# Kernel optimization log

Measured on AMD Instinct MI355X. Metric: run time of the kernel, lower is better.

## Reference

```python
import jax, jax.numpy as jnp
import numpy as np

N_HEADS = 8
EPS = 1e-5

def _mha(q_in, kv_in, wq, bq, wk, bk, wv, bv, wo, bo, causal):
    B, N, D = q_in.shape
    Dh = D // N_HEADS
    # projections (weights stored [in, out])
    Q = (q_in @ wq + bq).reshape(B, N, N_HEADS, Dh).swapaxes(1, 2)  # [B,H,N,Dh]
    K = (kv_in @ wk + bk).reshape(B, N, N_HEADS, Dh).swapaxes(1, 2)
    V = (kv_in @ wv + bv).reshape(B, N, N_HEADS, Dh).swapaxes(1, 2)
    scores = jnp.einsum('bhqd,bhkd->bhqk', Q, K) / jnp.sqrt(jnp.asarray(Dh, q_in.dtype))
    if causal:
        m = jnp.triu(jnp.ones((N, N), dtype=bool), k=1)
        scores = jnp.where(m, jnp.asarray(-jnp.inf, scores.dtype), scores)
    w = jax.nn.softmax(scores, axis=-1)
    attn = jnp.einsum('bhqk,bhkd->bhqd', w, V).swapaxes(1, 2).reshape(B, N, D)
    return attn @ wo + bo

def _ln(x, g, b):
    mu = jnp.mean(x, axis=-1, keepdims=True)
    var = jnp.var(x, axis=-1, keepdims=True)
    return (x - mu) / jnp.sqrt(var + EPS) * g + b

def setup_inputs() -> dict:
    key = jax.random.key(0)
    D, H, S = 512, 8, 4
    ks = jax.random.split(key, 32)
    def w(k, shape):
        return jax.random.normal(k, shape, dtype=jnp.float32) * 0.02
    inp = {
        'x': jax.random.normal(ks[0], (2, 2048, D), dtype=jnp.float32),
        'encoder_output': jax.random.normal(ks[1], (2, 2048, D), dtype=jnp.float32),
        # masked self-attention params
        'm_wq': w(ks[2], (D, D)), 'm_bq': jnp.zeros((D,), jnp.float32),
        'm_wk': w(ks[3], (D, D)), 'm_bk': jnp.zeros((D,), jnp.float32),
        'm_wv': w(ks[4], (D, D)), 'm_bv': jnp.zeros((D,), jnp.float32),
        'm_wo': w(ks[5], (D, D)), 'm_bo': jnp.zeros((D,), jnp.float32),
        # cross-attention params
        'c_wq': w(ks[6], (D, D)), 'c_bq': jnp.zeros((D,), jnp.float32),
        'c_wk': w(ks[7], (D, D)), 'c_bk': jnp.zeros((D,), jnp.float32),
        'c_wv': w(ks[8], (D, D)), 'c_bv': jnp.zeros((D,), jnp.float32),
        'c_wo': w(ks[9], (D, D)), 'c_bo': jnp.zeros((D,), jnp.float32),
        # layer norms
        'ln1_g': jnp.ones((D,), jnp.float32), 'ln1_b': jnp.zeros((D,), jnp.float32),
        'ln2_g': jnp.ones((D,), jnp.float32), 'ln2_b': jnp.zeros((D,), jnp.float32),
        'ln3_g': jnp.ones((D,), jnp.float32), 'ln3_b': jnp.zeros((D,), jnp.float32),
        # feed-forward (scale=4)
        'ff_w1': w(ks[10], (D, S * D)), 'ff_b1': jnp.zeros((S * D,), jnp.float32),
        'ff_w2': w(ks[11], (S * D, D)), 'ff_b2': jnp.zeros((D,), jnp.float32),
    }
    return inp

def reference(x, encoder_output,
              m_wq, m_bq, m_wk, m_bk, m_wv, m_bv, m_wo, m_bo,
              c_wq, c_bq, c_wk, c_bk, c_wv, c_bv, c_wo, c_bo,
              ln1_g, ln1_b, ln2_g, ln2_b, ln3_g, ln3_b,
              ff_w1, ff_b1, ff_w2, ff_b2):
    x = _mha(x, x, m_wq, m_bq, m_wk, m_bk, m_wv, m_bv, m_wo, m_bo, causal=True) + x
    x = _ln(x, ln1_g, ln1_b)
    x = _mha(x, encoder_output, c_wq, c_bq, c_wk, c_bk, c_wv, c_bv, c_wo, c_bo, causal=False) + x
    x = _ln(x, ln2_g, ln2_b)
    h = jax.nn.gelu(x @ ff_w1 + ff_b1, approximate=False)  # torch nn.GELU default = exact erf
    x = h @ ff_w2 + ff_b2 + x
    x = _ln(x, ln3_g, ln3_b)
    return x
```

## Files before the change

### kernel.cpp

```cpp
#include <hip/hip_runtime.h>
#include <hip/hip_bf16.h>

typedef __attribute__((ext_vector_type(8))) short short8;
typedef __attribute__((ext_vector_type(4))) float floatx4;
typedef unsigned short u16;
typedef unsigned int u32;

#define QSCALE 0.1803368801111244f

__device__ __forceinline__ u16 f2b(float f) {
    union { float f; u32 u; } v; v.f = f;
    u32 r = v.u + 0x7fffu + ((v.u >> 16) & 1u);
    return (u16)(r >> 16);
}

__device__ __forceinline__ float b2f(u16 b) {
    u32 u = ((u32)b) << 16;
    union { u32 u; float f; } v; v.u = u;
    return v.f;
}

__device__ __forceinline__ u32 pk2(float a, float b) {
    __hip_bfloat162 w = __float22bfloat162_rn(make_float2(a, b));
    return *(u32*)&w;
}

__device__ __forceinline__ float gelu_fast(float v) {
    float u = v * (0.7978845608028654f + 0.03567740814183367f * v * v);
    float t = exp2f(fminf(2.8853900817779268f * u, 80.f));
    return v * t * __builtin_amdgcn_rcpf(t + 1.f);
}

__device__ __forceinline__ void gload(const u16* g, u16* l) {
    __builtin_amdgcn_global_load_lds((const __attribute__((address_space(1))) void*)g,
                                     (__attribute__((address_space(3))) void*)l, 16, 0, 0);
}

struct TPent { const float* s; u16* d; int O; int dI; };
struct TP16 { TPent e[16]; };
__global__ __launch_bounds__(256) void transpose_convert16(TP16 p) {
    __shared__ float t[32][33];
    TPent e = p.e[blockIdx.z];
    int o0 = blockIdx.x * 32, i0 = blockIdx.y * 32;
    int tx = threadIdx.x, ty = threadIdx.y;
#pragma unroll
    for (int k = 0; k < 32; k += 8) t[ty + k][tx] = e.s[(size_t)(i0 + ty + k) * e.O + o0 + tx];
    __syncthreads();
#pragma unroll
    for (int k = 0; k < 32; k += 8) e.d[(size_t)(o0 + ty + k) * e.dI + i0 + tx] = f2b(t[tx][ty + k]);
}

__global__ __launch_bounds__(256) void gather_bias(const float* b0, const float* b1, const float* b2,
                                                   const float* b3, const float* b4,
                                                   float* dqkv, float* dkv) {
    int i = blockIdx.x * 256 + threadIdx.x;
    if      (i < 512)  dqkv[i] = b0[i];
    else if (i < 1024) dqkv[i] = b1[i - 512];
    else if (i < 1536) dqkv[i] = b2[i - 1024];
    else if (i < 2048) dkv[i - 1536] = b3[i - 1536];
    else               dkv[i - 1536] = b4[i - 2048];
}

__global__ __launch_bounds__(256) void cvt_bf16_2(const float4* __restrict__ s0, ushort4* __restrict__ d0,
                                                  const float4* __restrict__ s1, ushort4* __restrict__ d1) {
    int i = blockIdx.x * 256 + threadIdx.x;
    float4 v = s0[i];
    ushort4 o; o.x = f2b(v.x); o.y = f2b(v.y); o.z = f2b(v.z); o.w = f2b(v.w);
    d0[i] = o;
    v = s1[i];
    o.x = f2b(v.x); o.y = f2b(v.y); o.z = f2b(v.z); o.w = f2b(v.w);
    d1[i] = o;
}

__global__ __launch_bounds__(256) void gemm64x128(
    const u16* __restrict__ A, int lda,
    const u16* __restrict__ B, int ldb,
    int K,
    const float* __restrict__ bias,
    const float* __restrict__ residual,
    float* __restrict__ out_f, u16* __restrict__ out_b,
    int out_stride, int scale_ncols, int gelu_flag)
{
    __shared__ u16 lA[64 * 64];
    __shared__ u16 lB[128 * 64];
    int tid = threadIdx.x, wave = tid >> 6, lane = tid & 63;
    int g4 = lane >> 4, c16 = lane & 15;
    int swz = (c16 & 7) << 3;
    int bm = blockIdx.x * 64, bn = blockIdx.y * 128;
    int wm = (wave >> 1) * 32, wn = (wave & 1) * 64;
    int srow = tid >> 3, skseg = ((tid & 7) * 8) ^ ((srow & 7) << 3);
    const u16* Ar = A + (size_t)(bm + srow) * lda + skseg;
    const u16* Br = B + (size_t)(bn + srow) * ldb + skseg;
    size_t a32 = (size_t)32 * lda, b32 = (size_t)32 * ldb;

    floatx4 acc[2][4];
#pragma unroll
    for (int i = 0; i < 2; i++)
#pragma unroll
        for (int j = 0; j < 4; j++) acc[i][j] = (floatx4){0.f, 0.f, 0.f, 0.f};

    for (int kt = 0; kt < K; kt += 64) {
        __syncthreads();
        gload(Ar + kt,           lA + wave * 512);
        gload(Ar + kt + a32,     lA + 2048 + wave * 512);
        gload(Br + kt,           lB + wave * 512);
        gload(Br + kt + b32,     lB + 2048 + wave * 512);
        gload(Br + kt + 2 * b32, lB + 4096 + wave * 512);
        gload(Br + kt + 3 * b32, lB + 6144 + wave * 512);
        __syncthreads();
        short8 aF[2][2], bF[2][4];
#pragma unroll
        for (int kk = 0; kk < 2; kk++) {
            int ko = (g4 * 8 + kk * 32) ^ swz;
#pragma unroll
            for (int i = 0; i < 2; i++) aF[kk][i] = *(const short8*)&lA[(wm + i * 16 + c16) * 64 + ko];
#pragma unroll
            for (int j = 0; j < 4; j++) bF[kk][j] = *(const short8*)&lB[(wn + j * 16 + c16) * 64 + ko];
        }
#pragma unroll
        for (int kk = 0; kk < 2; kk++)
#pragma unroll
            for (int i = 0; i < 2; i++)
#pragma unroll
                for (int j = 0; j < 4; j++)
                    acc[i][j] = __builtin_amdgcn_mfma_f32_16x16x32_bf16(aF[kk][i], bF[kk][j], acc[i][j], 0, 0, 0);
    }

#pragma unroll
    for (int i = 0; i < 2; i++) {
        int row0 = bm + wm + i * 16 + g4 * 4;
#pragma unroll
        for (int j = 0; j < 4; j++) {
            int col = bn + wn + j * 16 + c16;
            float bv = bias[col];
#pragma unroll
            for (int r = 0; r < 4; r++) {
                int row = row0 + r;
                float v = acc[i][j][r] + bv;
                if (col < scale_ncols) v *= QSCALE;
                if (gelu_flag) v = gelu_fast(v);
                if (residual) v += residual[(size_t)row * out_stride + col];
                if (out_f) out_f[(size_t)row * out_stride + col] = v;
                else       out_b[(size_t)row * out_stride + col] = f2b(v);
            }
        }
    }
}

__global__ __launch_bounds__(256) void gemm64x128_dual(
    const u16* __restrict__ A0, const u16* __restrict__ B0, const float* __restrict__ bias0,
    u16* __restrict__ out0, int ostride0, int scale0,
    const u16* __restrict__ A1, const u16* __restrict__ B1, const float* __restrict__ bias1,
    u16* __restrict__ out1, int ostride1,
    int ys, int K, int lda, int ldb)
{
    __shared__ u16 lA[64 * 64];
    __shared__ u16 lB[128 * 64];
    int tid = threadIdx.x, wave = tid >> 6, lane = tid & 63;
    int g4 = lane >> 4, c16 = lane & 15;
    int swz = (c16 & 7) << 3;
    int by = blockIdx.y;
    const u16* A; const u16* B; const float* bias; u16* out; int ostride, scaleN, bn;
    if (by < ys) { A = A0; B = B0; bias = bias0; out = out0; ostride = ostride0; scaleN = scale0; bn = by * 128; }
    else         { A = A1; B = B1; bias = bias1; out = out1; ostride = ostride1; scaleN = 0;      bn = (by - ys) * 128; }
    int bm = blockIdx.x * 64;
    int wm = (wave >> 1) * 32, wn = (wave & 1) * 64;
    int srow = tid >> 3, skseg = ((tid & 7) * 8) ^ ((srow & 7) << 3);
    const u16* Ar = A + (size_t)(bm + srow) * lda + skseg;
    const u16* Br = B + (size_t)(bn + srow) * ldb + skseg;
    size_t a32 = (size_t)32 * lda, b32 = (size_t)32 * ldb;

    floatx4 acc[2][4];
#pragma unroll
    for (int i = 0; i < 2; i++)
#pragma unroll
        for (int j = 0; j < 4; j++) acc[i][j] = (floatx4){0.f, 0.f, 0.f, 0.f};

    for (int kt = 0; kt < K; kt += 64) {
        __syncthreads();
        gload(Ar + kt,           lA + wave * 512);
        gload(Ar + kt + a32,     lA + 2048 + wave * 512);
        gload(Br + kt,           lB + wave * 512);
        gload(Br + kt + b32,     lB + 2048 + wave * 512);
        gload(Br + kt + 2 * b32, lB + 4096 + wave * 512);
        gload(Br + kt + 3 * b32, lB + 6144 + wave * 512);
        __syncthreads();
        short8 aF[2][2], bF[2][4];
#pragma unroll
        for (int kk = 0; kk < 2; kk++) {
            int ko = (g4 * 8 + kk * 32) ^ swz;
#pragma unroll
            for (int i = 0; i < 2; i++) aF[kk][i] = *(const short8*)&lA[(wm + i * 16 + c16) * 64 + ko];
#pragma unroll
            for (int j = 0; j < 4; j++) bF[kk][j] = *(const short8*)&lB[(wn + j * 16 + c16) * 64 + ko];
        }
#pragma unroll
        for (int kk = 0; kk < 2; kk++)
#pragma unroll
            for (int i = 0; i < 2; i++)
#pragma unroll
                for (int j = 0; j < 4; j++)
                    acc[i][j] = __builtin_amdgcn_mfma_f32_16x16x32_bf16(aF[kk][i], bF[kk][j], acc[i][j], 0, 0, 0);
    }

#pragma unroll
    for (int i = 0; i < 2; i++) {
        int row0 = bm + wm + i * 16 + g4 * 4;
#pragma unroll
        for (int j = 0; j < 4; j++) {
            int col = bn + wn + j * 16 + c16;
            float bv = bias[col];
#pragma unroll
            for (int r = 0; r < 4; r++) {
                float v = acc[i][j][r] + bv;
                if (col < scaleN) v *= QSCALE;
                out[(size_t)(row0 + r) * ostride + col] = f2b(v);
            }
        }
    }
}

__global__ __launch_bounds__(256) void gemm64x64(
    const u16* __restrict__ A, int lda,
    const u16* __restrict__ B, int ldb,
    int K,
    const float* __restrict__ bias,
    u16* __restrict__ out_b,
    int out_stride, int scale_ncols)
{
    __shared__ u16 lA[64 * 64];
    __shared__ u16 lB[64 * 64];
    int tid = threadIdx.x, wave = tid >> 6, lane = tid & 63;
    int g4 = lane >> 4, c16 = lane & 15;
    int swz = (c16 & 7) << 3;
    int bm = blockIdx.x * 64, bn = blockIdx.y * 64;
    int wm = wave * 16;
    int srow = tid >> 3, skseg = ((tid & 7) * 8) ^ ((srow & 7) << 3);
    const u16* Ar = A + (size_t)(bm + srow) * lda + skseg;
    const u16* Br = B + (size_t)(bn + srow) * ldb + skseg;
    size_t a32 = (size_t)32 * lda, b32 = (size_t)32 * ldb;

    floatx4 acc[4];
#pragma unroll
    for (int j = 0; j < 4; j++) acc[j] = (floatx4){0.f, 0.f, 0.f, 0.f};

    for (int kt = 0; kt < K; kt += 64) {
        __syncthreads();
        gload(Ar + kt,       lA + wave * 512);
        gload(Ar + kt + a32, lA + 2048 + wave * 512);
        gload(Br + kt,       lB + wave * 512);
        gload(Br + kt + b32, lB + 2048 + wave * 512);
        __syncthreads();
        short8 aF[2], bF[2][4];
#pragma unroll
        for (int kk = 0; kk < 2; kk++) {
            int ko = (g4 * 8 + kk * 32) ^ swz;
            aF[kk] = *(const short8*)&lA[(wm + c16) * 64 + ko];
#pragma unroll
            for (int j = 0; j < 4; j++) bF[kk][j] = *(const short8*)&lB[(j * 16 + c16) * 64 + ko];
        }
#pragma unroll
        for (int kk = 0; kk < 2; kk++)
#pragma unroll
            for (int j = 0; j < 4; j++)
                acc[j] = __builtin_amdgcn_mfma_f32_16x16x32_bf16(aF[kk], bF[kk][j], acc[j], 0, 0, 0);
    }

    int row0 = bm + wm + g4 * 4;
#pragma unroll
    for (int j = 0; j < 4; j++) {
        int col = bn + j * 16 + c16;
        float bv = bias[col];
#pragma unroll
        for (int r = 0; r < 4; r++) {
            int row = row0 + r;
            float v = acc[j][r] + bv;
            if (col < scale_ncols) v *= QSCALE;
            out_b[(size_t)row * out_stride + col] = f2b(v);
        }
    }
}

__global__ __launch_bounds__(256) void gemm64x64s(
    const u16* __restrict__ A, int lda,
    const u16* __restrict__ B, int ldb,
    int Ksub,
    const float* __restrict__ bias,
    const float* __restrict__ res_f,
    const u16* __restrict__ res_b,
    u16* __restrict__ out0, int out_stride)
{
    __shared__ u16 lA[64 * 64];
    __shared__ u16 lB[64 * 64];
    int tid = threadIdx.x, wave = tid >> 6, lane = tid & 63;
    int g4 = lane >> 4, c16 = lane & 15;
    int swz = (c16 & 7) << 3;
    int bm = blockIdx.x * 64, bn = blockIdx.y * 64, sp = blockIdx.z;
    int wm = wave * 16;
    int srow = tid >> 3;
    int skseg = (((tid & 7) * 8) ^ ((srow & 7) << 3)) + sp * Ksub;
    const u16* Ar = A + (size_t)(bm + srow) * lda + skseg;
    const u16* Br = B + (size_t)(bn + srow) * ldb + skseg;
    size_t a32 = (size_t)32 * lda, b32 = (size_t)32 * ldb;

    floatx4 acc[4];
#pragma unroll
    for (int j = 0; j < 4; j++) acc[j] = (floatx4){0.f, 0.f, 0.f, 0.f};

    for (int kt = 0; kt < Ksub; kt += 64) {
        __syncthreads();
        gload(Ar + kt,       lA + wave * 512);
        gload(Ar + kt + a32, lA + 2048 + wave * 512);
        gload(Br + kt,       lB + wave * 512);
        gload(Br + kt + b32, lB + 2048 + wave * 512);
        __syncthreads();
        short8 aF[2], bF[2][4];
#pragma unroll
        for (int kk = 0; kk < 2; kk++) {
            int ko = (g4 * 8 + kk * 32) ^ swz;
            aF[kk] = *(const short8*)&lA[(wm + c16) * 64 + ko];
#pragma unroll
            for (int j = 0; j < 4; j++) bF[kk][j] = *(const short8*)&lB[(j * 16 + c16) * 64 + ko];
        }
#pragma unroll
        for (int kk = 0; kk < 2; kk++)
#pragma unroll
            for (int j = 0; j < 4; j++)
                acc[j] = __builtin_amdgcn_mfma_f32_16x16x32_bf16(aF[kk], bF[kk][j], acc[j], 0, 0, 0);
    }

    u16* out = out0 + (size_t)sp * 4096 * 512;
    int row0 = bm + wm + g4 * 4;
#pragma unroll
    for (int j = 0; j < 4; j++) {
        int col = bn + j * 16 + c16;
        float bv = (sp == 0) ? bias[col] : 0.f;
#pragma unroll
        for (int r = 0; r < 4; r++) {
            int row = row0 + r;
            float v = acc[j][r] + bv;
            if (sp == 0) {
                if (res_f)      v += res_f[(size_t)row * out_stride + col];
                else if (res_b) v += b2f(res_b[(size_t)row * out_stride + col]);
            }
            out[(size_t)row * out_stride + col] = f2b(v);
        }
    }
}


__global__ __launch_bounds__(256, 3) void attn_cross(
    const u16* __restrict__ Qp, int q_stride,
    const u16* __restrict__ Kp, int kv_stride,
    const u16* __restrict__ Vp,
    u16* __restrict__ Opart,
    float* __restrict__ Lpart)
{
    __shared__ u16 lK[64 * 72];
    __shared__ u16 lVT[64 * 72];
    int tid = threadIdx.x, wave = tid >> 6, lane = tid & 63;
    int g4 = lane >> 4, c16 = lane & 15;
    int id = blockIdx.x;
    int bh = (id & 7) | ((id >> 3 & 1) << 3);
    int rest = id >> 4;
    int qt = rest & 15;
    int sp = rest >> 4;
    size_t rowbase = (size_t)(bh >> 3) * 2048;
    int hoff = (bh & 7) * 64;
    const u16* Q = Qp + rowbase * q_stride + hoff;
    const u16* K = Kp + rowbase * kv_stride + hoff;
    const u16* V = Vp + rowbase * kv_stride + hoff;

    int qbase = qt * 128 + wave * 32;
    short8 qf[2][2];
#pragma unroll
    for (int qc = 0; qc < 2; qc++) {
        qf[qc][0] = *(const short8*)&Q[(size_t)(qbase + qc * 16 + c16) * q_stride + g4 * 8];
        qf[qc][1] = *(const short8*)&Q[(size_t)(qbase + qc * 16 + c16) * q_stride + g4 * 8 + 32];
    }

    int kr = tid >> 2, ks = (tid & 3) * 16;
    int krow = 16 * (2 * (kr >> 5) + ((kr >> 2) & 1)) + 4 * ((kr >> 3) & 3) + (kr & 3);
    const u16* Kbase = K + (size_t)kr * kv_stride + ks;
    int vk0 = (tid >> 3) * 2, vs = (tid & 7) * 8;
    const u16* Vbase = V + (size_t)vk0 * kv_stride + vs;

    int4 kv0, kv1, vv0, vv1;
    auto load_tile = [&](int kt) {
        const u16* kp = Kbase + (size_t)kt * 64 * kv_stride;
        kv0 = *(const int4*)(kp);
        kv1 = *(const int4*)(kp + 8);
        const u16* vp = Vbase + (size_t)kt * 64 * kv_stride;
        vv0 = *(const int4*)(vp);
        vv1 = *(const int4*)(vp + kv_stride);
    };
    auto store_tile = [&]() {
        *(int4*)&lK[krow * 72 + ks] = kv0;
        *(int4*)&lK[krow * 72 + ks + 8] = kv1;
        const u16* pa = (const u16*)&vv0;
        const u16* pb = (const u16*)&vv1;
#pragma unroll
        for (int j = 0; j < 8; j++) {
            int dh = vs + j;
            int keyS = vk0 ^ (((dh >> 3) & 3) << 4);
            u32 w = (u32)pa[j] | ((u32)pb[j] << 16);
            *(u32*)&lVT[dh * 72 + keyS] = w;
        }
    };

    floatx4 o[2][4];
#pragma unroll
    for (int qc = 0; qc < 2; qc++)
#pragma unroll
        for (int d = 0; d < 4; d++) o[qc][d] = (floatx4){0.f, 0.f, 0.f, 0.f};
    float ls0 = 0.f, ls1 = 0.f;

    int kt = sp;
    load_tile(kt);
    for (; kt < 32; kt += 4) {
        __syncthreads();
        store_tile();
        __syncthreads();
        if (kt + 4 < 32) load_tile(kt + 4);

        short8 b0[4], b1[4];
#pragma unroll
        for (int nt = 0; nt < 4; nt++) {
            b0[nt] = *(const short8*)&lK[(nt * 16 + c16) * 72 + g4 * 8];
            b1[nt] = *(const short8*)&lK[(nt * 16 + c16) * 72 + g4 * 8 + 32];
        }
        short8 pa[2][2];
#pragma unroll
        for (int qc = 0; qc < 2; qc++) {
            floatx4 sc[4];
#pragma unroll
            for (int nt = 0; nt < 4; nt++) {
                floatx4 z = (floatx4){0.f, 0.f, 0.f, 0.f};
                z = __builtin_amdgcn_mfma_f32_16x16x32_bf16(b0[nt], qf[qc][0], z, 0, 0, 0);
                z = __builtin_amdgcn_mfma_f32_16x16x32_bf16(b1[nt], qf[qc][1], z, 0, 0, 0);
                sc[nt] = z;
            }
            float e[4][4];
#pragma unroll
            for (int nt = 0; nt < 4; nt++)
#pragma unroll
                for (int r = 0; r < 4; r++) e[nt][r] = exp2f(sc[nt][r]);
            float s0 = (e[0][0] + e[0][1]) + (e[0][2] + e[0][3]);
            float s1 = (e[1][0] + e[1][1]) + (e[1][2] + e[1][3]);
            float s2 = (e[2][0] + e[2][1]) + (e[2][2] + e[2][3]);
            float s3 = (e[3][0] + e[3][1]) + (e[3][2] + e[3][3]);
            if (qc == 0) ls0 += (s0 + s1) + (s2 + s3);
            else         ls1 += (s0 + s1) + (s2 + s3);
            u32 w[8];
            w[0] = pk2(e[0][0], e[0][1]); w[1] = pk2(e[0][2], e[0][3]);
            w[2] = pk2(e[1][0], e[1][1]); w[3] = pk2(e[1][2], e[1][3]);
            w[4] = pk2(e[2][0], e[2][1]); w[5] = pk2(e[2][2], e[2][3]);
            w[6] = pk2(e[3][0], e[3][1]); w[7] = pk2(e[3][2], e[3][3]);
            pa[qc][0] = *(short8*)&w[0];
            pa[qc][1] = *(short8*)&w[4];
        }
#pragma unroll
        for (int d = 0; d < 4; d++) {
            int vswz = ((2 * d + (c16 >> 3)) & 3) << 4;
            short8 vb0 = *(const short8*)&lVT[(d * 16 + c16) * 72 + ((g4 * 8) ^ vswz)];
            short8 vb1 = *(const short8*)&lVT[(d * 16 + c16) * 72 + ((32 + g4 * 8) ^ vswz)];
            o[0][d] = __builtin_amdgcn_mfma_f32_16x16x32_bf16(pa[0][0], vb0, o[0][d], 0, 0, 0);
            o[0][d] = __builtin_amdgcn_mfma_f32_16x16x32_bf16(pa[0][1], vb1, o[0][d], 0, 0, 0);
            o[1][d] = __builtin_amdgcn_mfma_f32_16x16x32_bf16(pa[1][0], vb0, o[1][d], 0, 0, 0);
            o[1][d] = __builtin_amdgcn_mfma_f32_16x16x32_bf16(pa[1][1], vb1, o[1][d], 0, 0, 0);
        }
    }

    ls0 += __shfl_xor(ls0, 16); ls0 += __shfl_xor(ls0, 32);
    ls1 += __shfl_xor(ls1, 16); ls1 += __shfl_xor(ls1, 32);
    size_t slab = (size_t)(sp * 16 + bh) * 2048;
    if (g4 == 0) {
        Lpart[slab + qbase + c16] = ls0;
        Lpart[slab + qbase + 16 + c16] = ls1;
    }
#pragma unroll
    for (int qc = 0; qc < 2; qc++) {
        u16* Ob = Opart + (slab + qbase + qc * 16) * 64;
#pragma unroll
        for (int d = 0; d < 4; d++)
#pragma unroll
            for (int r = 0; r < 4; r++)
                Ob[(size_t)(4 * g4 + r) * 64 + d * 16 + c16] = f2b(o[qc][d][r]);
    }
}

__global__ __launch_bounds__(256, 2) void attn_causal_paired(
    const u16* __restrict__ Qp, int q_stride,
    const u16* __restrict__ Kp, int kv_stride,
    const u16* __restrict__ Vp,
    u16* __restrict__ Opart,
    float* __restrict__ Lpart)
{
    __shared__ u16 lK[64 * 72];
    __shared__ u16 lVT[64 * 72];
    int tid = threadIdx.x, wave = tid >> 6, lane = tid & 63;
    int g4 = lane >> 4, c16 = lane & 15;
    int id = blockIdx.x;
    int bh = (id & 7) | ((id >> 3 & 1) << 3);
    int rest = id >> 4;
    int p = rest & 7;
    int sp = rest >> 3;
    int TqA = p, TqB = 15 - p;
    int splitA = 2 * p + 2;
    size_t rowbase = (size_t)(bh >> 3) * 2048;
    int hoff = (bh & 7) * 64;
    const u16* Q = Qp + rowbase * q_stride + hoff;
    const u16* K = Kp + rowbase * kv_stride + hoff;
    const u16* V = Vp + rowbase * kv_stride + hoff;

    int qbA = TqA * 128 + wave * 32;
    int qbB = TqB * 128 + wave * 32;
    short8 qfA[2][2], qfB[2][2];
#pragma unroll
    for (int qc = 0; qc < 2; qc++) {
        qfA[qc][0] = *(const short8*)&Q[(size_t)(qbA + qc * 16 + c16) * q_stride + g4 * 8];
        qfA[qc][1] = *(const short8*)&Q[(size_t)(qbA + qc * 16 + c16) * q_stride + g4 * 8 + 32];
        qfB[qc][0] = *(const short8*)&Q[(size_t)(qbB + qc * 16 + c16) * q_stride + g4 * 8];
        qfB[qc][1] = *(const short8*)&Q[(size_t)(qbB + qc * 16 + c16) * q_stride + g4 * 8 + 32];
    }

    int kr = tid >> 2, ks = (tid & 3) * 16;
    int krow = 16 * (2 * (kr >> 5) + ((kr >> 2) & 1)) + 4 * ((kr >> 3) & 3) + (kr & 3);
    const u16* Kbase = K + (size_t)kr * kv_stride + ks;
    int vk0 = (tid >> 3) * 2, vs = (tid & 7) * 8;
    const u16* Vbase = V + (size_t)vk0 * kv_stride + vs;

    int4 kv0, kv1, vv0, vv1;
    auto load_tile = [&](int kt) {
        const u16* kp = Kbase + (size_t)kt * 64 * kv_stride;
        kv0 = *(const int4*)(kp);
        kv1 = *(const int4*)(kp + 8);
        const u16* vp = Vbase + (size_t)kt * 64 * kv_stride;
        vv0 = *(const int4*)(vp);
        vv1 = *(const int4*)(vp + kv_stride);
    };
    auto store_tile = [&]() {
        *(int4*)&lK[krow * 72 + ks] = kv0;
        *(int4*)&lK[krow * 72 + ks + 8] = kv1;
        const u16* pa_ = (const u16*)&vv0;
        const u16* pb_ = (const u16*)&vv1;
#pragma unroll
        for (int j = 0; j < 8; j++) {
            int dh = vs + j;
            int keyS = vk0 ^ (((dh >> 3) & 3) << 4);
            u32 w = (u32)pa_[j] | ((u32)pb_[j] << 16);
            *(u32*)&lVT[dh * 72 + keyS] = w;
        }
    };

    floatx4 oA[2][4], oB[2][4];
#pragma unroll
    for (int qc = 0; qc < 2; qc++)
#pragma unroll
        for (int d = 0; d < 4; d++) {
            oA[qc][d] = (floatx4){0.f, 0.f, 0.f, 0.f};
            oB[qc][d] = (floatx4){0.f, 0.f, 0.f, 0.f};
        }
    float lsA0 = 0.f, lsA1 = 0.f, lsB0 = 0.f, lsB1 = 0.f;

    auto compute_tile = [&](short8 (&qf)[2][2], floatx4 (&oacc)[2][4], float& l0, float& l1,
                            int qb, int kt, bool dg) {
        short8 b0[4], b1[4];
#pragma unroll
        for (int nt = 0; nt < 4; nt++) {
            b0[nt] = *(const short8*)&lK[(nt * 16 + c16) * 72 + g4 * 8];
            b1[nt] = *(const short8*)&lK[(nt * 16 + c16) * 72 + g4 * 8 + 32];
        }
        short8 pa[2][2];
#pragma unroll
        for (int qc = 0; qc < 2; qc++) {
            floatx4 sc[4];
#pragma unroll
            for (int nt = 0; nt < 4; nt++) {
                floatx4 z = (floatx4){0.f, 0.f, 0.f, 0.f};
                z = __builtin_amdgcn_mfma_f32_16x16x32_bf16(b0[nt], qf[qc][0], z, 0, 0, 0);
                z = __builtin_amdgcn_mfma_f32_16x16x32_bf16(b1[nt], qf[qc][1], z, 0, 0, 0);
                sc[nt] = z;
            }
            if (dg) {
                int qr = qb + qc * 16 + c16;
#pragma unroll
                for (int nt = 0; nt < 4; nt++) {
                    int key0 = kt * 64 + 8 * g4 + 4 * (nt & 1) + 32 * (nt >> 1);
#pragma unroll
                    for (int r = 0; r < 4; r++)
                        if (key0 + r > qr) sc[nt][r] = -1e30f;
                }
            }
            float e[4][4];
#pragma unroll
            for (int nt = 0; nt < 4; nt++)
#pragma unroll
                for (int r = 0; r < 4; r++) e[nt][r] = exp2f(sc[nt][r]);
            float s0 = (e[0][0] + e[0][1]) + (e[0][2] + e[0][3]);
            float s1 = (e[1][0] + e[1][1]) + (e[1][2] + e[1][3]);
            float s2 = (e[2][0] + e[2][1]) + (e[2][2] + e[2][3]);
            float s3 = (e[3][0] + e[3][1]) + (e[3][2] + e[3][3]);
            if (qc == 0) l0 += (s0 + s1) + (s2 + s3);
            else         l1 += (s0 + s1) + (s2 + s3);
            u32 w[8];
            w[0] = pk2(e[0][0], e[0][1]); w[1] = pk2(e[0][2], e[0][3]);
            w[2] = pk2(e[1][0], e[1][1]); w[3] = pk2(e[1][2], e[1][3]);
            w[4] = pk2(e[2][0], e[2][1]); w[5] = pk2(e[2][2], e[2][3]);
            w[6] = pk2(e[3][0], e[3][1]); w[7] = pk2(e[3][2], e[3][3]);
            pa[qc][0] = *(short8*)&w[0];
            pa[qc][1] = *(short8*)&w[4];
        }
#pragma unroll
        for (int d = 0; d < 4; d++) {
            int vswz = ((2 * d + (c16 >> 3)) & 3) << 4;
            short8 vb0 = *(const short8*)&lVT[(d * 16 + c16) * 72 + ((g4 * 8) ^ vswz)];
            short8 vb1 = *(const short8*)&lVT[(d * 16 + c16) * 72 + ((32 + g4 * 8) ^ vswz)];
            oacc[0][d] = __builtin_amdgcn_mfma_f32_16x16x32_bf16(pa[0][0], vb0, oacc[0][d], 0, 0, 0);
            oacc[0][d] = __builtin_amdgcn_mfma_f32_16x16x32_bf16(pa[0][1], vb1, oacc[0][d], 0, 0, 0);
            oacc[1][d] = __builtin_amdgcn_mfma_f32_16x16x32_bf16(pa[1][0], vb0, oacc[1][d], 0, 0, 0);
            oacc[1][d] = __builtin_amdgcn_mfma_f32_16x16x32_bf16(pa[1][1], vb1, oacc[1][d], 0, 0, 0);
        }
    };

    int t = sp;
    load_tile(t < splitA ? t : t - splitA);
    for (; t < 34; t += 4) {
        __syncthreads();
        store_tile();
        __syncthreads();
        if (t + 4 < 34) { int tn = t + 4; load_tile(tn < splitA ? tn : tn - splitA); }
        if (t < splitA) compute_tile(qfA, oA, lsA0, lsA1, qbA, t, t >= 2 * TqA);
        else {
            int kt = t - splitA;
            compute_tile(qfB, oB, lsB0, lsB1, qbB, kt, kt >= 2 * TqB);
        }
    }

    lsA0 += __shfl_xor(lsA0, 16); lsA0 += __shfl_xor(lsA0, 32);
    lsA1 += __shfl_xor(lsA1, 16); lsA1 += __shfl_xor(lsA1, 32);
    lsB0 += __shfl_xor(lsB0, 16); lsB0 += __shfl_xor(lsB0, 32);
    lsB1 += __shfl_xor(lsB1, 16); lsB1 += __shfl_xor(lsB1, 32);
    size_t slab = (size_t)(sp * 16 + bh) * 2048;
    if (g4 == 0) {
        Lpart[slab + qbA + c16] = lsA0;
        Lpart[slab + qbA + 16 + c16] = lsA1;
        Lpart[slab + qbB + c16] = lsB0;
        Lpart[slab + qbB + 16 + c16] = lsB1;
    }
#pragma unroll
    for (int qc = 0; qc < 2; qc++) {
        u16* ObA = Opart + (slab + qbA + qc * 16) * 64;
        u16* ObB = Opart + (slab + qbB + qc * 16) * 64;
#pragma unroll
        for (int d = 0; d < 4; d++)
#pragma unroll
            for (int r = 0; r < 4; r++) {
                ObA[(size_t)(4 * g4 + r) * 64 + d * 16 + c16] = f2b(oA[qc][d][r]);
                ObB[(size_t)(4 * g4 + r) * 64 + d * 16 + c16] = f2b(oB[qc][d][r]);
            }
    }
}

__global__ __launch_bounds__(256) void attn_combine(
    const ushort4* __restrict__ Op,
    const float* __restrict__ Lp,
    ushort4* __restrict__ out)
{
    int e = blockIdx.x * 256 + threadIdx.x;
    int dh4 = e & 15;
    int qrow = (e >> 4) & 2047;
    int bh = e >> 15;
    int li = bh * 2048 + qrow;
    float l = (Lp[li] + Lp[32768 + li]) + (Lp[65536 + li] + Lp[98304 + li]);
    float inv = 1.f / l;
    ushort4 a = Op[e];
    ushort4 b = Op[524288 + e];
    ushort4 c = Op[2 * 524288 + e];
    ushort4 d = Op[3 * 524288 + e];
    ushort4 o;
    o.x = f2b(((b2f(a.x) + b2f(b.x)) + (b2f(c.x) + b2f(d.x))) * inv);
    o.y = f2b(((b2f(a.y) + b2f(b.y)) + (b2f(c.y) + b2f(d.y))) * inv);
    o.z = f2b(((b2f(a.z) + b2f(b.z)) + (b2f(c.z) + b2f(d.z))) * inv);
    o.w = f2b(((b2f(a.w) + b2f(b.w)) + (b2f(c.w) + b2f(d.w))) * inv);
    int row = (bh >> 3) * 2048 + qrow;
    out[(size_t)row * 128 + (bh & 7) * 16 + dh4] = o;
}

__global__ __launch_bounds__(256) void ln_kernel(const u16* __restrict__ in0,
                                                 const u16* __restrict__ in1,
                                                 const float* __restrict__ g,
                                                 const float* __restrict__ b,
                                                 float* __restrict__ out_f,
                                                 u16* __restrict__ out_b)
{
    const int D = 512;
    int row = blockIdx.x, tid = threadIdx.x;
    size_t base = (size_t)row * D;
    float v0 = b2f(in0[base + tid]) + b2f(in1[base + tid]);
    float v1 = b2f(in0[base + tid + 256]) + b2f(in1[base + tid + 256]);
    float s = v0 + v1, ss = v0 * v0 + v1 * v1;
#pragma unroll
    for (int off = 1; off < 64; off <<= 1) { s += __shfl_xor(s, off); ss += __shfl_xor(ss, off); }
    __shared__ float red[8];
    int wave = tid >> 6, lane = tid & 63;
    if (lane == 0) { red[wave] = s; red[4 + wave] = ss; }
    __syncthreads();
    float st = red[0] + red[1] + red[2] + red[3];
    float sst = red[4] + red[5] + red[6] + red[7];
    float mu = st * (1.f / 512.f);
    float var = sst * (1.f / 512.f) - mu * mu;
    float rs = rsqrtf(var + 1e-5f);
    float y0 = (v0 - mu) * rs * g[tid] + b[tid];
    float y1 = (v1 - mu) * rs * g[tid + 256] + b[tid + 256];
    if (out_f) { out_f[base + tid] = y0; out_f[base + tid + 256] = y1; }
    if (out_b) { out_b[base + tid] = f2b(y0); out_b[base + tid + 256] = f2b(y1); }
}

extern "C" void kernel_launch(void* const* d_in, const int* in_sizes, int n_in,
                              void* d_out, int out_size, void* d_ws, size_t ws_size,
                              hipStream_t stream)
{
    (void)in_sizes; (void)n_in; (void)out_size; (void)ws_size;
    const float* x     = (const float*)d_in[0];
    const float* enc   = (const float*)d_in[1];
    const float* m_wq  = (const float*)d_in[2];  const float* m_bq = (const float*)d_in[3];
    const float* m_wk  = (const float*)d_in[4];  const float* m_bk = (const float*)d_in[5];
    const float* m_wv  = (const float*)d_in[6];  const float* m_bv = (const float*)d_in[7];
    const float* m_wo  = (const float*)d_in[8];  const float* m_bo = (const float*)d_in[9];
    const float* c_wq  = (const float*)d_in[10]; const float* c_bq = (const float*)d_in[11];
    const float* c_wk  = (const float*)d_in[12]; const float* c_bk = (const float*)d_in[13];
    const float* c_wv  = (const float*)d_in[14]; const float* c_bv = (const float*)d_in[15];
    const float* c_wo  = (const float*)d_in[16]; const float* c_bo = (const float*)d_in[17];
    const float* ln1_g = (const float*)d_in[18]; const float* ln1_b = (const float*)d_in[19];
    const float* ln2_g = (const float*)d_in[20]; const float* ln2_b = (const float*)d_in[21];
    const float* ln3_g = (const float*)d_in[22]; const float* ln3_b = (const float*)d_in[23];
    const float* ff_w1 = (const float*)d_in[24]; const float* ff_b1 = (const float*)d_in[25];
    const float* ff_w2 = (const float*)d_in[26]; const float* ff_b2 = (const float*)d_in[27];

    char* base = (char*)d_ws; size_t off = 0;
    auto alloc = [&](size_t bytes) -> void* {
        void* p = base + off; off = (off + bytes + 255) & ~(size_t)255; return p;
    };
    u16*   Wqkv_m = (u16*)alloc(1536 * 512 * 2);
    u16*   Wo_m   = (u16*)alloc(512 * 512 * 2);
    u16*   Wq_c   = (u16*)alloc(512 * 512 * 2);
    u16*   Wkv_c  = (u16*)alloc(1024 * 512 * 2);
    u16*   Wo_c   = (u16*)alloc(512 * 512 * 2);
    u16*   W1t    = (u16*)alloc(2048 * 512 * 2);
    u16*   W2t    = (u16*)alloc(512 * 2048 * 2);
    float* bqkv_m = (float*)alloc(1536 * 4);
    float* bkv_c  = (float*)alloc(1024 * 4);
    u16*   xb     = (u16*)alloc((size_t)4096 * 512 * 2);
    u16*   encb   = (u16*)alloc((size_t)4096 * 512 * 2);
    u16*   qkvm   = (u16*)alloc((size_t)4096 * 1536 * 2);
    u16*   attnm  = (u16*)alloc((size_t)4096 * 512 * 2);
    u16*   y01    = (u16*)alloc((size_t)2 * 4096 * 512 * 2);
    u16*   x1b    = (u16*)alloc((size_t)4096 * 512 * 2);
    u16*   qc     = (u16*)alloc((size_t)4096 * 512 * 2);
    u16*   kvc    = (u16*)alloc((size_t)4096 * 1024 * 2);
    u16*   attnc  = (u16*)alloc((size_t)4096 * 512 * 2);
    u16*   x2b    = (u16*)alloc((size_t)4096 * 512 * 2);
    u16*   h      = (u16*)alloc((size_t)4096 * 2048 * 2);
    u16*   Opart  = (u16*)alloc((size_t)4 * 16 * 2048 * 64 * 2);
    float* Lpart  = (float*)alloc((size_t)4 * 16 * 2048 * 4);

    TP16 tp;
    tp.e[0] = {m_wq, Wqkv_m,              512, 512};
    tp.e[1] = {m_wk, Wqkv_m + 512 * 512,  512, 512};
    tp.e[2] = {m_wv, Wqkv_m + 1024 * 512, 512, 512};
    tp.e[3] = {m_wo, Wo_m,                512, 512};
    tp.e[4] = {c_wq, Wq_c,                512, 512};
    tp.e[5] = {c_wk, Wkv_c,               512, 512};
    tp.e[6] = {c_wv, Wkv_c + 512 * 512,   512, 512};
    tp.e[7] = {c_wo, Wo_c,                512, 512};
    for (int k = 0; k < 4; k++)
        tp.e[8 + k]  = {ff_w1 + 512 * k,        W1t + k * 512 * 512, 2048, 512};
    for (int k = 0; k < 4; k++)
        tp.e[12 + k] = {ff_w2 + (size_t)512 * k * 512, W2t + 512 * k, 512, 2048};
    transpose_convert16<<<dim3(16, 16, 16), dim3(32, 8), 0, stream>>>(tp);
    gather_bias<<<10, 256, 0, stream>>>(m_bq, m_bk, m_bv, c_bk, c_bv, bqkv_m, bkv_c);
    cvt_bf16_2<<<2048, 256, 0, stream>>>((const float4*)x, (ushort4*)xb,
                                         (const float4*)enc, (ushort4*)encb);

    gemm64x128_dual<<<dim3(64, 20), 256, 0, stream>>>(
        xb, Wqkv_m, bqkv_m, qkvm, 1536, 512,
        encb, Wkv_c, bkv_c, kvc, 1024,
        12, 512, 512, 512);

    attn_causal_paired<<<512, 256, 0, stream>>>(qkvm, 1536, qkvm + 512, 1536, qkvm + 1024,
                                                Opart, Lpart);
    attn_combine<<<2048, 256, 0, stream>>>((const ushort4*)Opart, Lpart, (ushort4*)attnm);
    gemm64x64s<<<dim3(64, 8, 2), 256, 0, stream>>>(attnm, 512, Wo_m, 512, 256,
                                                   m_bo, x, nullptr, y01, 512);
    ln_kernel<<<4096, 256, 0, stream>>>(y01, y01 + (size_t)4096 * 512, ln1_g, ln1_b,
                                        nullptr, x1b);

    gemm64x64<<<dim3(64, 8), 256, 0, stream>>>(x1b, 512, Wq_c, 512, 512,
                                               c_bq, qc, 512, 512);
    attn_cross<<<1024, 256, 0, stream>>>(qc, 512, kvc, 1024, kvc + 512,
                                         Opart, Lpart);
    attn_combine<<<2048, 256, 0, stream>>>((const ushort4*)Opart, Lpart, (ushort4*)attnc);
    gemm64x64s<<<dim3(64, 8, 2), 256, 0, stream>>>(attnc, 512, Wo_c, 512, 256,
                                                   c_bo, nullptr, x1b, y01, 512);
    ln_kernel<<<4096, 256, 0, stream>>>(y01, y01 + (size_t)4096 * 512, ln2_g, ln2_b,
                                        nullptr, x2b);

    gemm64x128<<<dim3(64, 16), 256, 0, stream>>>(x2b, 512, W1t, 512, 512,
                                                 ff_b1, nullptr, nullptr, h, 2048, 0, 1);
    gemm64x64s<<<dim3(64, 8, 2), 256, 0, stream>>>(h, 2048, W2t, 2048, 1024,
                                                   ff_b2, nullptr, x2b, y01, 512);
    ln_kernel<<<4096, 256, 0, stream>>>(y01, y01 + (size_t)4096 * 512, ln3_g, ln3_b,
                                        (float*)d_out, nullptr);
}
```

Baseline: 294.2 us.

## Fuse split-KV attention combine into output projection GEMM A-tile load

Removes the separate attn_combine kernel and folds the partial-output reduction and softmax normalization into the Wo projection GEMM. Each GEMM block reads the four bf16 partial outputs and partial row sums, normalizes them, and writes the bf16 A tile directly into LDS. This drops a kernel launch and the write and re-read of the combined attention tensor for both attention blocks. In exchange, each A tile is recomputed by all 8 column blocks, so partial outputs are read redundantly, and loading A through registers replaces the direct global-to-LDS load.

```diff
diff --git a/kernel.cpp b/kernel.cpp
--- a/kernel.cpp
+++ b/kernel.cpp
@@ -311,6 +311,98 @@
         __syncthreads();
         gload(Ar + kt,       lA + wave * 512);
         gload(Ar + kt + a32, lA + 2048 + wave * 512);
+        gload(Br + kt,       lB + wave * 512);
+        gload(Br + kt + b32, lB + 2048 + wave * 512);
+        __syncthreads();
+        short8 aF[2], bF[2][4];
+#pragma unroll
+        for (int kk = 0; kk < 2; kk++) {
+            int ko = (g4 * 8 + kk * 32) ^ swz;
+            aF[kk] = *(const short8*)&lA[(wm + c16) * 64 + ko];
+#pragma unroll
+            for (int j = 0; j < 4; j++) bF[kk][j] = *(const short8*)&lB[(j * 16 + c16) * 64 + ko];
+        }
+#pragma unroll
+        for (int kk = 0; kk < 2; kk++)
+#pragma unroll
+            for (int j = 0; j < 4; j++)
+                acc[j] = __builtin_amdgcn_mfma_f32_16x16x32_bf16(aF[kk], bF[kk][j], acc[j], 0, 0, 0);
+    }
+
+    u16* out = out0 + (size_t)sp * 4096 * 512;
+    int row0 = bm + wm + g4 * 4;
+#pragma unroll
+    for (int j = 0; j < 4; j++) {
+        int col = bn + j * 16 + c16;
+        float bv = (sp == 0) ? bias[col] : 0.f;
+#pragma unroll
+        for (int r = 0; r < 4; r++) {
+            int row = row0 + r;
+            float v = acc[j][r] + bv;
+            if (sp == 0) {
+                if (res_f)      v += res_f[(size_t)row * out_stride + col];
+                else if (res_b) v += b2f(res_b[(size_t)row * out_stride + col]);
+            }
+            out[(size_t)row * out_stride + col] = f2b(v);
+        }
+    }
+}
+
+__global__ __launch_bounds__(256) void gemm_wo_fused(
+    const u16* __restrict__ Opart,
+    const float* __restrict__ Lpart,
+    const u16* __restrict__ B, int ldb,
+    const float* __restrict__ bias,
+    const float* __restrict__ res_f,
+    const u16* __restrict__ res_b,
+    u16* __restrict__ out0, int out_stride)
+{
+    __shared__ u16 lA[64 * 64];
+    __shared__ u16 lB[64 * 64];
+    int tid = threadIdx.x, wave = tid >> 6, lane = tid & 63;
+    int g4 = lane >> 4, c16 = lane & 15;
+    int swz = (c16 & 7) << 3;
+    int bm = blockIdx.x * 64, bn = blockIdx.y * 64, sp = blockIdx.z;
+    int wm = wave * 16;
+    int b = bm >> 11, q0 = bm & 2047;
+    int srow = tid >> 3;
+    int skseg = (((tid & 7) * 8) ^ ((srow & 7) << 3)) + sp * 256;
+    const u16* Br = B + (size_t)(bn + srow) * ldb + skseg;
+    size_t b32 = (size_t)32 * ldb;
+    int ar = tid >> 2, j0 = (tid & 3) * 16;
+    int arow = q0 + ar;
+    int wa0 = ar * 64 + (j0 ^ ((ar & 7) << 3));
+    int wa1 = ar * 64 + ((j0 + 8) ^ ((ar & 7) << 3));
+
+    floatx4 acc[4];
+#pragma unroll
+    for (int j = 0; j < 4; j++) acc[j] = (floatx4){0.f, 0.f, 0.f, 0.f};
+
+    for (int kt = 0; kt < 256; kt += 64) {
+        int h = (sp * 256 + kt) >> 6;
+        int bh = b * 8 + h;
+        float va[16];
+#pragma unroll
+        for (int t = 0; t < 16; t++) va[t] = 0.f;
+        float L = 0.f;
+#pragma unroll
+        for (int s = 0; s < 4; s++) {
+            const u16* src = Opart + ((size_t)((s * 16 + bh) * 2048 + arow)) * 64 + j0;
+            int4 p0 = *(const int4*)(src);
+            int4 p1 = *(const int4*)(src + 8);
+            const u16* e0 = (const u16*)&p0;
+            const u16* e1 = (const u16*)&p1;
+#pragma unroll
+            for (int t = 0; t < 8; t++) { va[t] += b2f(e0[t]); va[8 + t] += b2f(e1[t]); }
+            L += Lpart[(size_t)(s * 16 + bh) * 2048 + arow];
+        }
+        float inv = 1.f / L;
+        u32 w[8];
+#pragma unroll
+        for (int t = 0; t < 8; t++) w[t] = pk2(va[2 * t] * inv, va[2 * t + 1] * inv);
+        __syncthreads();
+        *(int4*)&lA[wa0] = *(int4*)&w[0];
+        *(int4*)&lA[wa1] = *(int4*)&w[4];
         gload(Br + kt,       lB + wave * 512);
         gload(Br + kt + b32, lB + 2048 + wave * 512);
         __syncthreads();
@@ -662,31 +754,6 @@
     }
 }
 
-__global__ __launch_bounds__(256) void attn_combine(
-    const ushort4* __restrict__ Op,
-    const float* __restrict__ Lp,
-    ushort4* __restrict__ out)
-{
-    int e = blockIdx.x * 256 + threadIdx.x;
-    int dh4 = e & 15;
-    int qrow = (e >> 4) & 2047;
-    int bh = e >> 15;
-    int li = bh * 2048 + qrow;
-    float l = (Lp[li] + Lp[32768 + li]) + (Lp[65536 + li] + Lp[98304 + li]);
-    float inv = 1.f / l;
-    ushort4 a = Op[e];
-    ushort4 b = Op[524288 + e];
-    ushort4 c = Op[2 * 524288 + e];
-    ushort4 d = Op[3 * 524288 + e];
-    ushort4 o;
-    o.x = f2b(((b2f(a.x) + b2f(b.x)) + (b2f(c.x) + b2f(d.x))) * inv);
-    o.y = f2b(((b2f(a.y) + b2f(b.y)) + (b2f(c.y) + b2f(d.y))) * inv);
-    o.z = f2b(((b2f(a.z) + b2f(b.z)) + (b2f(c.z) + b2f(d.z))) * inv);
-    o.w = f2b(((b2f(a.w) + b2f(b.w)) + (b2f(c.w) + b2f(d.w))) * inv);
-    int row = (bh >> 3) * 2048 + qrow;
-    out[(size_t)row * 128 + (bh & 7) * 16 + dh4] = o;
-}
-
 __global__ __launch_bounds__(256) void ln_kernel(const u16* __restrict__ in0,
                                                  const u16* __restrict__ in1,
                                                  const float* __restrict__ g,
@@ -754,12 +821,10 @@
     u16*   xb     = (u16*)alloc((size_t)4096 * 512 * 2);
     u16*   encb   = (u16*)alloc((size_t)4096 * 512 * 2);
     u16*   qkvm   = (u16*)alloc((size_t)4096 * 1536 * 2);
-    u16*   attnm  = (u16*)alloc((size_t)4096 * 512 * 2);
     u16*   y01    = (u16*)alloc((size_t)2 * 4096 * 512 * 2);
     u16*   x1b    = (u16*)alloc((size_t)4096 * 512 * 2);
     u16*   qc     = (u16*)alloc((size_t)4096 * 512 * 2);
     u16*   kvc    = (u16*)alloc((size_t)4096 * 1024 * 2);
-    u16*   attnc  = (u16*)alloc((size_t)4096 * 512 * 2);
     u16*   x2b    = (u16*)alloc((size_t)4096 * 512 * 2);
     u16*   h      = (u16*)alloc((size_t)4096 * 2048 * 2);
     u16*   Opart  = (u16*)alloc((size_t)4 * 16 * 2048 * 64 * 2);
@@ -790,9 +855,8 @@
 
     attn_causal_paired<<<512, 256, 0, stream>>>(qkvm, 1536, qkvm + 512, 1536, qkvm + 1024,
                                                 Opart, Lpart);
-    attn_combine<<<2048, 256, 0, stream>>>((const ushort4*)Opart, Lpart, (ushort4*)attnm);
-    gemm64x64s<<<dim3(64, 8, 2), 256, 0, stream>>>(attnm, 512, Wo_m, 512, 256,
-                                                   m_bo, x, nullptr, y01, 512);
+    gemm_wo_fused<<<dim3(64, 8, 2), 256, 0, stream>>>(Opart, Lpart, Wo_m, 512,
+                                                      m_bo, x, nullptr, y01, 512);
     ln_kernel<<<4096, 256, 0, stream>>>(y01, y01 + (size_t)4096 * 512, ln1_g, ln1_b,
                                         nullptr, x1b);
 
@@ -800,9 +864,8 @@
                                                c_bq, qc, 512, 512);
     attn_cross<<<1024, 256, 0, stream>>>(qc, 512, kvc, 1024, kvc + 512,
                                          Opart, Lpart);
-    attn_combine<<<2048, 256, 0, stream>>>((const ushort4*)Opart, Lpart, (ushort4*)attnc);
-    gemm64x64s<<<dim3(64, 8, 2), 256, 0, stream>>>(attnc, 512, Wo_c, 512, 256,
-                                                   c_bo, nullptr, x1b, y01, 512);
+    gemm_wo_fused<<<dim3(64, 8, 2), 256, 0, stream>>>(Opart, Lpart, Wo_c, 512,
+                                                      c_bo, nullptr, x1b, y01, 512);
     ln_kernel<<<4096, 256, 0, stream>>>(y01, y01 + (size_t)4096 * 512, ln2_g, ln2_b,
                                         nullptr, x2b);
 
```

New measurement: 302.7 us. +2.9%, slower.
